# Kernel optimization log

Measured on AMD Instinct MI355X. Metric: run time of the kernel, lower is better.

The kernel has to match this reference:

```python
import jax, jax.numpy as jnp
import numpy as np

BBOX_POS_MAX = 1024.0
BN_EPS = 1e-5


def _bn_eval(x, g, b, rm, rv):
    # BatchNorm1d in eval mode: affine transform with running stats
    return g * (x - rm) * jax.lax.rsqrt(rv + BN_EPS) + b


def setup_inputs() -> dict:
    key = jax.random.key(0)
    ks = jax.random.split(key, 24)
    B, N, F = 32, 512, 1024
    E = 32768
    H1, H2, H3 = 512, 256, 128          # node_pred_hidden
    EH1, EH2 = 64, 64                   # edge_pred_hidden
    NC, EC = 8, 10                      # node/edge concept channels
    BC = 9                              # bbox_channels (4 bbox + 4 dir + 1 prio)
    s = 0.02
    inp = {
        'roi_features': jax.random.normal(ks[0], (B, N, F), jnp.float32),
        'batch_bboxes': jax.random.uniform(ks[1], (B, N, 4), jnp.float32) * BBOX_POS_MAX,
        'batch_directions': jax.random.uniform(ks[2], (B, N, 4), jnp.float32),
        'batch_priorities': jax.random.uniform(ks[3], (B, N), jnp.float32),
        'batch_edge_index': jax.random.randint(ks[4], (B, 2, E), 0, N, jnp.int32),
        # node_predictor params
        'np_w1': jax.random.normal(ks[5], (F, H1), jnp.float32) * s,
        'np_b1': jnp.zeros((H1,), jnp.float32),
        'bn1_g': jnp.ones((H1,), jnp.float32),
        'bn1_b': jnp.zeros((H1,), jnp.float32),
        'bn1_rm': jnp.zeros((H1,), jnp.float32),
        'bn1_rv': jnp.ones((H1,), jnp.float32),
        'np_w2': jax.random.normal(ks[6], (H1, H2), jnp.float32) * s,
        'np_b2': jnp.zeros((H2,), jnp.float32),
        'bn2_g': jnp.ones((H2,), jnp.float32),
        'bn2_b': jnp.zeros((H2,), jnp.float32),
        'bn2_rm': jnp.zeros((H2,), jnp.float32),
        'bn2_rv': jnp.ones((H2,), jnp.float32),
        'np_w3': jax.random.normal(ks[7], (H2, H3), jnp.float32) * s,
        'np_b3': jnp.zeros((H3,), jnp.float32),
        'ni_w': jax.random.normal(ks[8], (H3, NC), jnp.float32) * s,
        'ni_b': jnp.zeros((NC,), jnp.float32),
        # edge_predictor params (input dim = 2 * bbox_channels)
        'ep_w1': jax.random.normal(ks[9], (2 * BC, EH1), jnp.float32) * s,
        'ep_b1': jnp.zeros((EH1,), jnp.float32),
        'ep_w2': jax.random.normal(ks[10], (EH1, EH2), jnp.float32) * s,
        'ep_b2': jnp.zeros((EH2,), jnp.float32),
        'ei_w': jax.random.normal(ks[11], (EH2, EC), jnp.float32) * s,
        'ei_b': jnp.zeros((EC,), jnp.float32),
    }
    return inp


def reference(roi_features, batch_bboxes, batch_directions, batch_priorities,
              batch_edge_index,
              np_w1, np_b1, bn1_g, bn1_b, bn1_rm, bn1_rv,
              np_w2, np_b2, bn2_g, bn2_b, bn2_rm, bn2_rv,
              np_w3, np_b3, ni_w, ni_b,
              ep_w1, ep_b1, ep_w2, ep_b2, ei_w, ei_b):
    B, N, F = roi_features.shape
    # ---- node path: MLP (eval-mode BN, dropout = identity) + sigmoid interpreter
    x = roi_features.reshape(B * N, F)
    h = jax.nn.relu(_bn_eval(x @ np_w1 + np_b1, bn1_g, bn1_b, bn1_rm, bn1_rv))
    h = jax.nn.relu(_bn_eval(h @ np_w2 + np_b2, bn2_g, bn2_b, bn2_rm, bn2_rv))
    h = jax.nn.relu(h @ np_w3 + np_b3)
    node_concepts = jax.nn.sigmoid(h @ ni_w + ni_b).reshape(B, N, -1)
    # ---- edge path: per-batch gather of node attrs via edge_index, concat, MLP
    node_attr = jnp.concatenate(
        [batch_bboxes / BBOX_POS_MAX, batch_directions, batch_priorities[..., None]],
        axis=-1)  # [B, N, 9]
    C = node_attr.shape[-1]
    src_idx = batch_edge_index[:, 0, :, None]  # [B, E, 1]
    dst_idx = batch_edge_index[:, 1, :, None]
    src = jnp.take_along_axis(node_attr, src_idx.astype(jnp.int32), axis=1)  # [B, E, 9]
    dst = jnp.take_along_axis(node_attr, dst_idx.astype(jnp.int32), axis=1)
    edge_attr = jnp.concatenate([src, dst], axis=-1).reshape(-1, 2 * C)  # [B*E, 18]
    e = jax.nn.relu(edge_attr @ ep_w1 + ep_b1)
    e = jax.nn.relu(e @ ep_w2 + ep_b2)
    edge_concepts = jax.nn.sigmoid(e @ ei_w + ei_b)  # [B*E, EC]
    return node_concepts, edge_concepts
```

## Files before the change

### kernel.cpp

```cpp
#include <hip/hip_runtime.h>
#include <cstdint>
#include <cstddef>

#define BN_EPSF 1e-5f

constexpr int B_  = 32, N_ = 512, F_ = 1024, E_ = 32768;
constexpr int H1_ = 512, H2_ = 256, H3_ = 128, NC_ = 8, EC_ = 10;
constexpr int M_  = B_ * N_;
constexpr int NE_ = B_ * E_;

typedef short bf16x8 __attribute__((ext_vector_type(8)));
typedef float f32x4  __attribute__((ext_vector_type(4)));

__device__ __forceinline__ short f2bf(float f) {
  union { float f; unsigned u; } v; v.f = f;
  unsigned r = v.u + 0x7fffu + ((v.u >> 16) & 1u);
  return (short)(r >> 16);
}
__device__ __forceinline__ unsigned rnepack(float a, float b) {
  unsigned ua = __float_as_uint(a); ua = ua + 0x7fffu + ((ua >> 16) & 1u);
  unsigned ub = __float_as_uint(b); ub = ub + 0x7fffu + ((ub >> 16) & 1u);
  return __builtin_amdgcn_perm(ub, ua, 0x07060302u);
}

#define GLDS(gp, lp) __builtin_amdgcn_global_load_lds( \
    (const __attribute__((address_space(1))) void*)(gp), \
    (__attribute__((address_space(3))) void*)(lp), 16, 0, 0)

#define MFMA(a, b, c) __builtin_amdgcn_mfma_f32_16x16x32_bf16((a), (b), (c), 0, 0, 0)

__device__ __forceinline__ void wt_body(
    const float* __restrict__ W, short* __restrict__ Wt, int K, int N,
    int bx, int by, float (*s)[33])
{
  const int tx = threadIdx.x & 31, ty = threadIdx.x >> 5;
  const int k0 = by * 32, n0 = bx * 32;
#pragma unroll
  for (int r = 0; r < 4; r++)
    s[ty * 4 + r][tx] = W[(size_t)(k0 + ty * 4 + r) * N + n0 + tx];
  __syncthreads();
#pragma unroll
  for (int r = 0; r < 4; r++)
    Wt[(size_t)(n0 + ty * 4 + r) * K + k0 + tx] = f2bf(s[tx][ty * 4 + r]);
}

__global__ __launch_bounds__(256) void k_prep(
    const float* __restrict__ roi, ushort* __restrict__ roiB,
    const float* __restrict__ w1, short* __restrict__ w1t,
    const float* __restrict__ w2, short* __restrict__ w2t,
    const float* __restrict__ w3, short* __restrict__ w3t,
    const float* __restrict__ bbox, const float* __restrict__ dir,
    const float* __restrict__ pri, float* __restrict__ na)
{
  __shared__ float s[32][33];
  const int bx = blockIdx.x;
  if (bx < 8192) {
    int i = bx * 256 + threadIdx.x;
    float4 a = *(const float4*)(roi + (size_t)i * 8);
    float4 b = *(const float4*)(roi + (size_t)i * 8 + 4);
    unsigned o[4];
    o[0] = rnepack(a.x, a.y); o[1] = rnepack(a.z, a.w);
    o[2] = rnepack(b.x, b.y); o[3] = rnepack(b.z, b.w);
    *(uint4*)(roiB + (size_t)i * 8) = *(uint4*)o;
  } else if (bx < 8704) {
    int idx = bx - 8192; wt_body(w1, w1t, F_, H1_, idx & 15, idx >> 4, s);
  } else if (bx < 8832) {
    int idx = bx - 8704; wt_body(w2, w2t, H1_, H2_, idx & 7, idx >> 3, s);
  } else if (bx < 8864) {
    int idx = bx - 8832; wt_body(w3, w3t, H2_, H3_, idx & 3, idx >> 2, s);
  } else {
    int i = (bx - 8864) * 256 + threadIdx.x;
    float4 b = *(const float4*)(bbox + (size_t)i * 4);
    float4 d = *(const float4*)(dir + (size_t)i * 4);
    float p = pri[i];
    const float inv = 1.0f / 1024.0f;
    float* o = na + (size_t)i * 12;
    *(float4*)(o + 0) = make_float4(b.x * inv, b.y * inv, b.z * inv, b.w * inv);
    *(float4*)(o + 4) = make_float4(d.x, d.y, d.z, d.w);
    *(float4*)(o + 8) = make_float4(p, 0.f, 0.f, 0.f);
  }
}

__global__ __launch_bounds__(256) void k_gemm_l1(
    const short* __restrict__ A, const short* __restrict__ Wt,
    const float* __restrict__ bias,
    const float* __restrict__ g, const float* __restrict__ bb,
    const float* __restrict__ rm, const float* __restrict__ rv,
    short* __restrict__ C, int M, int K, int N)
{
  __shared__ short As[128 * 32];
  __shared__ short Bs[128 * 32];

  const int tid  = threadIdx.x;
  const int wave = tid >> 6, lane = tid & 63;
  const int m0 = blockIdx.y * 128, n0 = blockIdx.x * 128;
  const int wm = wave >> 1, wn = wave & 1;

  const int arow = tid >> 2;
  const int akq  = (tid & 3) * 8;

  f32x4 acc[4][4] = {};

  for (int k0 = 0; k0 < K; k0 += 32) {
#pragma unroll
    for (int it = 0; it < 2; it++)
      GLDS(A + (size_t)(m0 + it * 64 + arow) * K + k0 + akq,
           (char*)As + it * 4096 + wave * 1024);
#pragma unroll
    for (int it = 0; it < 2; it++)
      GLDS(Wt + (size_t)(n0 + it * 64 + arow) * K + k0 + akq,
           (char*)Bs + it * 4096 + wave * 1024);
    __syncthreads();

    const int ko = (lane >> 4) * 8;
    bf16x8 af[4], bfr[4];
#pragma unroll
    for (int t = 0; t < 4; t++) {
      af[t]  = *(const bf16x8*)&As[(wm * 64 + t * 16 + (lane & 15)) * 32 + ko];
      bfr[t] = *(const bf16x8*)&Bs[(wn * 64 + t * 16 + (lane & 15)) * 32 + ko];
    }
#pragma unroll
    for (int ti = 0; ti < 4; ti++)
#pragma unroll
      for (int tj = 0; tj < 4; tj++)
        acc[ti][tj] = MFMA(af[ti], bfr[tj], acc[ti][tj]);
    __syncthreads();
  }

#pragma unroll
  for (int tj = 0; tj < 4; tj++) {
    const int col = n0 + wn * 64 + tj * 16 + (lane & 15);
    const float bi = bias[col];
    float s = g[col] * rsqrtf(rv[col] + BN_EPSF);
    float t = bb[col] - rm[col] * s;
#pragma unroll
    for (int ti = 0; ti < 4; ti++) {
      const int rbase = m0 + wm * 64 + ti * 16 + ((lane >> 4) << 2);
#pragma unroll
      for (int r = 0; r < 4; r++) {
        float v = fmaf(acc[ti][tj][r] + bi, s, t);
        C[(size_t)(rbase + r) * N + col] = f2bf(fmaxf(v, 0.f));
      }
    }
  }
}

__global__ __launch_bounds__(256) void k_tail(
    const short* __restrict__ h1, const short* __restrict__ w2t,
    const short* __restrict__ w3t,
    const float* __restrict__ b2, const float* __restrict__ g2,
    const float* __restrict__ bb2, const float* __restrict__ rm2,
    const float* __restrict__ rv2,
    const float* __restrict__ b3, const float* __restrict__ niw,
    const float* __restrict__ nib, float* __restrict__ out)
{
  __shared__ __align__(16) char arena[53760];
  short* sA  = (short*)arena;
  short* sB  = (short*)(arena + 4096);
  short* sH2 = (short*)(arena + 36864);
  short* sB3 = (short*)arena;
  short* sH3 = (short*)(arena + 16384);

  const int tid  = threadIdx.x;
  const int wave = tid >> 6, lane = tid & 63;
  const int lm = lane & 15, q = lane >> 4;
  const int wm = wave >> 1, wn = wave & 1;
  const int m0 = blockIdx.x * 32;
  const int srow = tid >> 2;
  const int skq  = (tid & 3) * 8;

  f32x4 acc2[8] = {};
  for (int k0 = 0; k0 < 512; k0 += 64) {
    {
      int c = tid >> 7, row = (tid >> 2) & 31;
      GLDS(h1 + (size_t)(m0 + row) * 512 + k0 + c * 32 + skq,
           (char*)sA + wave * 1024);
    }
#pragma unroll
    for (int it = 0; it < 4; it++)
#pragma unroll
      for (int c = 0; c < 2; c++)
        GLDS(w2t + (size_t)(it * 64 + srow) * 512 + k0 + c * 32 + skq,
             (char*)sB + c * 16384 + it * 4096 + wave * 1024);
    __syncthreads();
#pragma unroll
    for (int c = 0; c < 2; c++) {
      bf16x8 af = *(const bf16x8*)&sA[c * 1024 + (wm * 16 + lm) * 32 + q * 8];
#pragma unroll
      for (int nt = 0; nt < 8; nt++) {
        bf16x8 bfr = *(const bf16x8*)&sB[c * 8192 + (wn * 128 + nt * 16 + lm) * 32 + q * 8];
        acc2[nt] = MFMA(af, bfr, acc2[nt]);
      }
    }
    __syncthreads();
  }
#pragma unroll
  for (int nt = 0; nt < 8; nt++) {
    int col = wn * 128 + nt * 16 + lm;
    float s = g2[col] * rsqrtf(rv2[col] + BN_EPSF);
    float t = bb2[col] - rm2[col] * s;
    float bi = b2[col];
#pragma unroll
    for (int r = 0; r < 4; r++) {
      float v = fmaf(acc2[nt][r] + bi, s, t);
      sH2[(wm * 16 + q * 4 + r) * 264 + col] = f2bf(fmaxf(v, 0.f));
    }
  }
  __syncthreads();

  f32x4 acc3[4] = {};
  for (int k0 = 0; k0 < 256; k0 += 64) {
#pragma unroll
    for (int it = 0; it < 2; it++)
#pragma unroll
      for (int c = 0; c < 2; c++)
        GLDS(w3t + (size_t)(it * 64 + srow) * 256 + k0 + c * 32 + skq,
             (char*)sB3 + c * 8192 + it * 4096 + wave * 1024);
    __syncthreads();
#pragma unroll
    for (int c = 0; c < 2; c++) {
      bf16x8 af = *(const bf16x8*)&sH2[(wm * 16 + lm) * 264 + k0 + c * 32 + q * 8];
#pragma unroll
      for (int nt = 0; nt < 4; nt++) {
        bf16x8 bfr = *(const bf16x8*)&sB3[c * 4096 + (wn * 64 + nt * 16 + lm) * 32 + q * 8];
        acc3[nt] = MFMA(af, bfr, acc3[nt]);
      }
    }
    __syncthreads();
  }
#pragma unroll
  for (int nt = 0; nt < 4; nt++) {
    int col = wn * 64 + nt * 16 + lm;
    float bi = b3[col];
#pragma unroll
    for (int r = 0; r < 4; r++) {
      float v = acc3[nt][r] + bi;
      sH3[(wm * 16 + q * 4 + r) * 136 + col] = f2bf(fmaxf(v, 0.f));
    }
  }
  __syncthreads();

  if (wave < 2) {
    f32x4 a4 = {};
#pragma unroll
    for (int c = 0; c < 4; c++) {
      ushort tmp[8];
#pragma unroll
      for (int j = 0; j < 8; j++) {
        int k = c * 32 + q * 8 + j;
        tmp[j] = (lm < 8) ? (ushort)f2bf(niw[k * 8 + lm]) : (ushort)0;
      }
      bf16x8 fw = *(bf16x8*)tmp;
      bf16x8 af4 = *(const bf16x8*)&sH3[(wave * 16 + lm) * 136 + c * 32 + q * 8];
      a4 = MFMA(af4, fw, a4);
    }
    if (lm < 8) {
      float bi = nib[lm];
#pragma unroll
      for (int r = 0; r < 4; r++) {
        float v = a4[r] + bi;
        out[(size_t)(m0 + wave * 16 + q * 4 + r) * 8 + lm] = 1.f / (1.f + __expf(-v));
      }
    }
  }
}

__global__ __launch_bounds__(256, 2) void k_edge_mfma(
    const float* __restrict__ na, const int* __restrict__ eidx,
    const float* __restrict__ w1, const float* __restrict__ b1,
    const float* __restrict__ w2, const float* __restrict__ b2,
    const float* __restrict__ wo, const float* __restrict__ bo,
    float* __restrict__ out)
{
  __shared__ __align__(16) short sA[9216];
  __shared__ __align__(16) short sH1[128 * 72];
  __shared__ float sB[144];

  const int tid  = threadIdx.x;
  const int wave = tid >> 6, lane = tid & 63;
  const int lm  = lane & 15;
  const int lk8 = (lane >> 4) * 8;
  const int lr  = (lane >> 4) * 4;

  short* sW1 = sA;
  short* sW2 = sA + 2048;
  short* sW3 = sA + 6144;
  short* sX  = sA;
  short* sH2 = sA;

  for (int i = tid; i < 2048; i += 256) {
    int n = i >> 5, k = i & 31;
    sW1[i] = (k < 18) ? f2bf(w1[k * 64 + n]) : (short)0;
  }
  for (int i = tid; i < 4096; i += 256) {
    int n = i >> 6, k = i & 63;
    sW2[i] = f2bf(w2[k * 64 + n]);
  }
  for (int i = tid; i < 1024; i += 256) {
    int n = i >> 6, k = i & 63;
    sW3[i] = (n < 10) ? f2bf(wo[k * 10 + n]) : (short)0;
  }
  if (tid < 64) { sB[tid] = b1[tid]; sB[64 + tid] = b2[tid]; }
  if (tid < 16) sB[128 + tid] = (tid < 10) ? bo[tid] : 0.f;
  __syncthreads();

  bf16x8 fW1[4], fW2[4][2], fW3[2];
#pragma unroll
  for (int t = 0; t < 4; t++)
    fW1[t] = *(const bf16x8*)&sW1[(t * 16 + lm) * 32 + lk8];
#pragma unroll
  for (int t = 0; t < 4; t++)
#pragma unroll
    for (int ks = 0; ks < 2; ks++)
      fW2[t][ks] = *(const bf16x8*)&sW2[(t * 16 + lm) * 64 + ks * 32 + lk8];
#pragma unroll
  for (int ks = 0; ks < 2; ks++)
    fW3[ks] = *(const bf16x8*)&sW3[lm * 64 + ks * 32 + lk8];
  float bias1v[4], bias2v[4];
#pragma unroll
  for (int t = 0; t < 4; t++) {
    bias1v[t] = sB[t * 16 + lm];
    bias2v[t] = sB[64 + t * 16 + lm];
  }
  const float biasOv = sB[128 + lm];
  __syncthreads();

  for (int bi = 0; bi < 4; bi++) {
    const int e0 = (blockIdx.x * 4 + bi) * 128;

    if (tid < 128) {
      int e = e0 + tid;
      int b = e >> 15, kk = e & (E_ - 1);
      const int* ei = eidx + (size_t)b * 2 * E_;
      int s = ei[kk], d = ei[E_ + kk];
      const float* ps = na + ((size_t)b * N_ + s) * 12;
      const float* pd = na + ((size_t)b * N_ + d) * 12;
      float4 a0 = *(const float4*)(ps);
      float4 a1 = *(const float4*)(ps + 4);
      float  a2 = ps[8];
      float4 c0 = *(const float4*)(pd);
      float4 c1 = *(const float4*)(pd + 4);
      float  c2 = pd[8];
      ushort xr[32];
      xr[0] = (ushort)f2bf(a0.x); xr[1] = (ushort)f2bf(a0.y);
      xr[2] = (ushort)f2bf(a0.z); xr[3] = (ushort)f2bf(a0.w);
      xr[4] = (ushort)f2bf(a1.x); xr[5] = (ushort)f2bf(a1.y);
      xr[6] = (ushort)f2bf(a1.z); xr[7] = (ushort)f2bf(a1.w);
      xr[8] = (ushort)f2bf(a2);
      xr[9]  = (ushort)f2bf(c0.x); xr[10] = (ushort)f2bf(c0.y);
      xr[11] = (ushort)f2bf(c0.z); xr[12] = (ushort)f2bf(c0.w);
      xr[13] = (ushort)f2bf(c1.x); xr[14] = (ushort)f2bf(c1.y);
      xr[15] = (ushort)f2bf(c1.z); xr[16] = (ushort)f2bf(c1.w);
      xr[17] = (ushort)f2bf(c2);
#pragma unroll
      for (int i = 18; i < 32; i++) xr[i] = 0;
      ushort* row = (ushort*)&sX[tid * 40];
      *(uint4*)(row + 0)  = *(uint4*)&xr[0];
      *(uint4*)(row + 8)  = *(uint4*)&xr[8];
      *(uint4*)(row + 16) = *(uint4*)&xr[16];
      *(uint4*)(row + 24) = *(uint4*)&xr[24];
    }
    __syncthreads();

    bf16x8 a1f[2];
#pragma unroll
    for (int ti = 0; ti < 2; ti++)
      a1f[ti] = *(const bf16x8*)&sX[(wave * 32 + ti * 16 + lm) * 40 + lk8];
    f32x4 acc1[2][4] = {};
#pragma unroll
    for (int ti = 0; ti < 2; ti++)
#pragma unroll
      for (int tj = 0; tj < 4; tj++)
        acc1[ti][tj] = MFMA(a1f[ti], fW1[tj], acc1[ti][tj]);
#pragma unroll
    for (int ti = 0; ti < 2; ti++)
#pragma unroll
      for (int tj = 0; tj < 4; tj++)
#pragma unroll
        for (int r = 0; r < 4; r++) {
          int row = wave * 32 + ti * 16 + lr + r;
          float v = acc1[ti][tj][r] + bias1v[tj];
          sH1[row * 72 + tj * 16 + lm] = f2bf(fmaxf(v, 0.f));
        }
    __syncthreads();

    bf16x8 a2f[2][2];
#pragma unroll
    for (int ti = 0; ti < 2; ti++)
#pragma unroll
      for (int ks = 0; ks < 2; ks++)
        a2f[ti][ks] = *(const bf16x8*)&sH1[(wave * 32 + ti * 16 + lm) * 72 + ks * 32 + lk8];
    f32x4 acc2[2][4] = {};
#pragma unroll
    for (int ks = 0; ks < 2; ks++)
#pragma unroll
      for (int ti = 0; ti < 2; ti++)
#pragma unroll
        for (int tj = 0; tj < 4; tj++)
          acc2[ti][tj] = MFMA(a2f[ti][ks], fW2[tj][ks], acc2[ti][tj]);
#pragma unroll
    for (int ti = 0; ti < 2; ti++)
#pragma unroll
      for (int tj = 0; tj < 4; tj++)
#pragma unroll
        for (int r = 0; r < 4; r++) {
          int row = wave * 32 + ti * 16 + lr + r;
          float v = acc2[ti][tj][r] + bias2v[tj];
          sH2[row * 72 + tj * 16 + lm] = f2bf(fmaxf(v, 0.f));
        }

    bf16x8 a3f[2][2];
#pragma unroll
    for (int ti = 0; ti < 2; ti++)
#pragma unroll
      for (int ks = 0; ks < 2; ks++)
        a3f[ti][ks] = *(const bf16x8*)&sH2[(wave * 32 + ti * 16 + lm) * 72 + ks * 32 + lk8];
    f32x4 acc3[2] = {};
#pragma unroll
    for (int ks = 0; ks < 2; ks++)
#pragma unroll
      for (int ti = 0; ti < 2; ti++)
        acc3[ti] = MFMA(a3f[ti][ks], fW3[ks], acc3[ti]);
    if (lm < 10) {
#pragma unroll
      for (int ti = 0; ti < 2; ti++)
#pragma unroll
        for (int r = 0; r < 4; r++) {
          int row = wave * 32 + ti * 16 + lr + r;
          float v = acc3[ti][r] + biasOv;
          out[(size_t)(e0 + row) * 10 + lm] = 1.f / (1.f + __expf(-v));
        }
    }
    __syncthreads();
  }
}

extern "C" void kernel_launch(void* const* d_in, const int* in_sizes, int n_in,
                              void* d_out, int out_size, void* d_ws, size_t ws_size,
                              hipStream_t stream)
{
  const float* roi   = (const float*)d_in[0];
  const float* bbox  = (const float*)d_in[1];
  const float* dir   = (const float*)d_in[2];
  const float* pri   = (const float*)d_in[3];
  const int*   eidx  = (const int*)d_in[4];
  const float* w1    = (const float*)d_in[5];
  const float* b1    = (const float*)d_in[6];
  const float* g1    = (const float*)d_in[7];
  const float* bb1   = (const float*)d_in[8];
  const float* rm1   = (const float*)d_in[9];
  const float* rv1   = (const float*)d_in[10];
  const float* w2    = (const float*)d_in[11];
  const float* b2    = (const float*)d_in[12];
  const float* g2    = (const float*)d_in[13];
  const float* bb2   = (const float*)d_in[14];
  const float* rm2   = (const float*)d_in[15];
  const float* rv2   = (const float*)d_in[16];
  const float* w3    = (const float*)d_in[17];
  const float* b3    = (const float*)d_in[18];
  const float* niw   = (const float*)d_in[19];
  const float* nib   = (const float*)d_in[20];
  const float* ew1   = (const float*)d_in[21];
  const float* eb1   = (const float*)d_in[22];
  const float* ew2   = (const float*)d_in[23];
  const float* eb2   = (const float*)d_in[24];
  const float* eow   = (const float*)d_in[25];
  const float* eob   = (const float*)d_in[26];

  float* out_node = (float*)d_out;
  float* out_edge = (float*)d_out + (size_t)M_ * NC_;

  char* w = (char*)d_ws;
  short*  roiB = (short*)w;
  short*  w1t  = (short*)(w + 33554432);
  short*  w2t  = (short*)(w + 34603008);
  short*  w3t  = (short*)(w + 34865152);
  float*  na   = (float*)(w + 34930688);
  short*  h1   = (short*)(w + 35717120);

  k_prep<<<8928, 256, 0, stream>>>(roi, (ushort*)roiB, w1, w1t, w2, w2t,
                                   w3, w3t, bbox, dir, pri, na);

  k_edge_mfma<<<NE_ / 512, 256, 0, stream>>>(
      na, eidx, ew1, eb1, ew2, eb2, eow, eob, out_edge);

  k_gemm_l1<<<dim3(H1_ / 128, M_ / 128), 256, 0, stream>>>(
      roiB, w1t, b1, g1, bb1, rm1, rv1, h1, M_, F_, H1_);
  k_tail<<<M_ / 32, 256, 0, stream>>>(
      h1, w2t, w3t, b2, g2, bb2, rm2, rv2, b3, niw, nib, out_node);
}
```

Measured before the change: 267.8 us.

## Fuse edge MLP and layer-1 GEMM into one interleaved launch with LDS node attrs

The separate edge-MLP kernel and layer-1 GEMM kernel are merged into one launch of 1536 blocks. Every third block computes a 128x128 GEMM tile, and the other two each process 1024 edges of a single batch. Edge blocks now build that batch's bf16 node attributes in LDS straight from bbox/dir/priority, which removes the node-attribute precompute in k_prep and its global scratch buffer. The aim is to overlap the memory- and latency-bound edge work with the MFMA-bound GEMM and cut one launch and a global round trip. The cost is that each edge block redoes the weight and attribute setup, and the mixed blocks share one 3-per-CU occupancy limit.

```diff
diff --git a/kernel.cpp b/kernel.cpp
--- a/kernel.cpp
+++ b/kernel.cpp
@@ -48,9 +48,7 @@
     const float* __restrict__ roi, ushort* __restrict__ roiB,
     const float* __restrict__ w1, short* __restrict__ w1t,
     const float* __restrict__ w2, short* __restrict__ w2t,
-    const float* __restrict__ w3, short* __restrict__ w3t,
-    const float* __restrict__ bbox, const float* __restrict__ dir,
-    const float* __restrict__ pri, float* __restrict__ na)
+    const float* __restrict__ w3, short* __restrict__ w3t)
 {
   __shared__ float s[32][33];
   const int bx = blockIdx.x;
@@ -66,82 +64,258 @@
     int idx = bx - 8192; wt_body(w1, w1t, F_, H1_, idx & 15, idx >> 4, s);
   } else if (bx < 8832) {
     int idx = bx - 8704; wt_body(w2, w2t, H1_, H2_, idx & 7, idx >> 3, s);
-  } else if (bx < 8864) {
+  } else {
     int idx = bx - 8832; wt_body(w3, w3t, H2_, H3_, idx & 3, idx >> 2, s);
-  } else {
-    int i = (bx - 8864) * 256 + threadIdx.x;
-    float4 b = *(const float4*)(bbox + (size_t)i * 4);
-    float4 d = *(const float4*)(dir + (size_t)i * 4);
-    float p = pri[i];
-    const float inv = 1.0f / 1024.0f;
-    float* o = na + (size_t)i * 12;
-    *(float4*)(o + 0) = make_float4(b.x * inv, b.y * inv, b.z * inv, b.w * inv);
-    *(float4*)(o + 4) = make_float4(d.x, d.y, d.z, d.w);
-    *(float4*)(o + 8) = make_float4(p, 0.f, 0.f, 0.f);
-  }
-}
-
-__global__ __launch_bounds__(256) void k_gemm_l1(
-    const short* __restrict__ A, const short* __restrict__ Wt,
-    const float* __restrict__ bias,
-    const float* __restrict__ g, const float* __restrict__ bb,
-    const float* __restrict__ rm, const float* __restrict__ rv,
-    short* __restrict__ C, int M, int K, int N)
+  }
+}
+
+__global__ __launch_bounds__(256, 3) void k_fused(
+    const float* __restrict__ bbox, const float* __restrict__ dir,
+    const float* __restrict__ pri, const int* __restrict__ eidx,
+    const float* __restrict__ ew1, const float* __restrict__ eb1,
+    const float* __restrict__ ew2, const float* __restrict__ eb2,
+    const float* __restrict__ eow, const float* __restrict__ eob,
+    float* __restrict__ out_edge,
+    const short* __restrict__ roiB, const short* __restrict__ w1t,
+    const float* __restrict__ b1, const float* __restrict__ g1,
+    const float* __restrict__ bb1, const float* __restrict__ rm1,
+    const float* __restrict__ rv1, short* __restrict__ h1)
 {
-  __shared__ short As[128 * 32];
-  __shared__ short Bs[128 * 32];
-
+  __shared__ __align__(16) char arena[49728];
+
+  const int bx = blockIdx.x;
+  const int rsel = bx % 3;
   const int tid  = threadIdx.x;
   const int wave = tid >> 6, lane = tid & 63;
-  const int m0 = blockIdx.y * 128, n0 = blockIdx.x * 128;
-  const int wm = wave >> 1, wn = wave & 1;
-
-  const int arow = tid >> 2;
-  const int akq  = (tid & 3) * 8;
-
-  f32x4 acc[4][4] = {};
-
-  for (int k0 = 0; k0 < K; k0 += 32) {
-#pragma unroll
-    for (int it = 0; it < 2; it++)
-      GLDS(A + (size_t)(m0 + it * 64 + arow) * K + k0 + akq,
-           (char*)As + it * 4096 + wave * 1024);
-#pragma unroll
-    for (int it = 0; it < 2; it++)
-      GLDS(Wt + (size_t)(n0 + it * 64 + arow) * K + k0 + akq,
-           (char*)Bs + it * 4096 + wave * 1024);
-    __syncthreads();
-
-    const int ko = (lane >> 4) * 8;
-    bf16x8 af[4], bfr[4];
-#pragma unroll
-    for (int t = 0; t < 4; t++) {
-      af[t]  = *(const bf16x8*)&As[(wm * 64 + t * 16 + (lane & 15)) * 32 + ko];
-      bfr[t] = *(const bf16x8*)&Bs[(wn * 64 + t * 16 + (lane & 15)) * 32 + ko];
-    }
-#pragma unroll
-    for (int ti = 0; ti < 4; ti++)
+  const int lm = lane & 15;
+
+  if (rsel == 2) {
+    const int lb = bx / 3;
+    short* As = (short*)arena;
+    short* Bs = (short*)(arena + 8192);
+    const int m0 = (lb >> 2) * 128, n0 = (lb & 3) * 128;
+    const int wm = wave >> 1, wn = wave & 1;
+    const int arow = tid >> 2;
+    const int akq  = (tid & 3) * 8;
+
+    f32x4 acc[4][4] = {};
+    for (int k0 = 0; k0 < F_; k0 += 32) {
+#pragma unroll
+      for (int it = 0; it < 2; it++)
+        GLDS(roiB + (size_t)(m0 + it * 64 + arow) * F_ + k0 + akq,
+             (char*)As + it * 4096 + wave * 1024);
+#pragma unroll
+      for (int it = 0; it < 2; it++)
+        GLDS(w1t + (size_t)(n0 + it * 64 + arow) * F_ + k0 + akq,
+             (char*)Bs + it * 4096 + wave * 1024);
+      __syncthreads();
+
+      const int ko = (lane >> 4) * 8;
+      bf16x8 af[4], bfr[4];
+#pragma unroll
+      for (int t = 0; t < 4; t++) {
+        af[t]  = *(const bf16x8*)&As[(wm * 64 + t * 16 + lm) * 32 + ko];
+        bfr[t] = *(const bf16x8*)&Bs[(wn * 64 + t * 16 + lm) * 32 + ko];
+      }
+#pragma unroll
+      for (int ti = 0; ti < 4; ti++)
+#pragma unroll
+        for (int tj = 0; tj < 4; tj++)
+          acc[ti][tj] = MFMA(af[ti], bfr[tj], acc[ti][tj]);
+      __syncthreads();
+    }
+#pragma unroll
+    for (int tj = 0; tj < 4; tj++) {
+      const int col = n0 + wn * 64 + tj * 16 + lm;
+      const float bi = b1[col];
+      float s = g1[col] * rsqrtf(rv1[col] + BN_EPSF);
+      float t = bb1[col] - rm1[col] * s;
+#pragma unroll
+      for (int ti = 0; ti < 4; ti++) {
+        const int rbase = m0 + wm * 64 + ti * 16 + ((lane >> 4) << 2);
+#pragma unroll
+        for (int r = 0; r < 4; r++) {
+          float v = fmaf(acc[ti][tj][r] + bi, s, t);
+          h1[(size_t)(rbase + r) * H1_ + col] = f2bf(fmaxf(v, 0.f));
+        }
+      }
+    }
+    return;
+  }
+
+  const int eb = (bx / 3) * 2 + rsel;
+  const int batch = eb >> 5;
+  const int e_base = eb * 1024;
+
+  short* sA    = (short*)arena;
+  short* sH1   = (short*)(arena + 18432);
+  ushort* sAttr= (ushort*)(arena + 36864);
+  float* sB    = (float*)(arena + 49152);
+
+  short* sW1 = sA;
+  short* sW2 = sA + 2048;
+  short* sW3 = sA + 6144;
+  short* sX  = sA;
+  short* sH2 = sA;
+
+  const int lk8 = (lane >> 4) * 8;
+  const int lr  = (lane >> 4) * 4;
+
+  for (int i = tid; i < 2048; i += 256) {
+    int n = i >> 5, k = i & 31;
+    sW1[i] = (k < 18) ? f2bf(ew1[k * 64 + n]) : (short)0;
+  }
+  for (int i = tid; i < 4096; i += 256) {
+    int n = i >> 6, k = i & 63;
+    sW2[i] = f2bf(ew2[k * 64 + n]);
+  }
+  for (int i = tid; i < 1024; i += 256) {
+    int n = i >> 6, k = i & 63;
+    sW3[i] = (n < 10) ? f2bf(eow[k * 10 + n]) : (short)0;
+  }
+  if (tid < 64) { sB[tid] = eb1[tid]; sB[64 + tid] = eb2[tid]; }
+  if (tid < 16) sB[128 + tid] = (tid < 10) ? eob[tid] : 0.f;
+  {
+    const float inv = 1.0f / 1024.0f;
+    for (int n = tid; n < 512; n += 256) {
+      int gi = batch * 512 + n;
+      float4 bv = *(const float4*)(bbox + (size_t)gi * 4);
+      float4 dv = *(const float4*)(dir + (size_t)gi * 4);
+      float pp = pri[gi];
+      unsigned* row = (unsigned*)&sAttr[n * 12];
+      uint2 a, c, e;
+      a.x = rnepack(bv.x * inv, bv.y * inv); a.y = rnepack(bv.z * inv, bv.w * inv);
+      c.x = rnepack(dv.x, dv.y);             c.y = rnepack(dv.z, dv.w);
+      e.x = rnepack(pp, 0.f);                e.y = 0;
+      *(uint2*)(row + 0) = a; *(uint2*)(row + 2) = c; *(uint2*)(row + 4) = e;
+    }
+  }
+  __syncthreads();
+
+  bf16x8 fW1[4], fW2[4][2], fW3[2];
+#pragma unroll
+  for (int t = 0; t < 4; t++)
+    fW1[t] = *(const bf16x8*)&sW1[(t * 16 + lm) * 32 + lk8];
+#pragma unroll
+  for (int t = 0; t < 4; t++)
+#pragma unroll
+    for (int ks = 0; ks < 2; ks++)
+      fW2[t][ks] = *(const bf16x8*)&sW2[(t * 16 + lm) * 64 + ks * 32 + lk8];
+#pragma unroll
+  for (int ks = 0; ks < 2; ks++)
+    fW3[ks] = *(const bf16x8*)&sW3[lm * 64 + ks * 32 + lk8];
+  float bias1v[4], bias2v[4];
+#pragma unroll
+  for (int t = 0; t < 4; t++) {
+    bias1v[t] = sB[t * 16 + lm];
+    bias2v[t] = sB[64 + t * 16 + lm];
+  }
+  const float biasOv = sB[128 + lm];
+  __syncthreads();
+
+  const int* ei = eidx + (size_t)batch * 2 * E_;
+
+  for (int bi = 0; bi < 8; bi++) {
+    const int e0 = e_base + bi * 128;
+
+    if (tid < 128) {
+      int kk = (e0 + tid) & (E_ - 1);
+      int s = ei[kk], d = ei[E_ + kk];
+      const unsigned* ps = (const unsigned*)&sAttr[s * 12];
+      const unsigned* pd = (const unsigned*)&sAttr[d * 12];
+      uint2 s01 = *(const uint2*)(ps);
+      uint2 s23 = *(const uint2*)(ps + 2);
+      uint2 s45 = *(const uint2*)(ps + 4);
+      uint2 d01 = *(const uint2*)(pd);
+      uint2 d23 = *(const uint2*)(pd + 2);
+      uint2 d45 = *(const uint2*)(pd + 4);
+      unsigned x[16];
+      x[0] = s01.x; x[1] = s01.y; x[2] = s23.x; x[3] = s23.y;
+      x[4] = (s45.x & 0xffffu) | (d01.x << 16);
+      x[5] = (d01.x >> 16) | (d01.y << 16);
+      x[6] = (d01.y >> 16) | (d23.x << 16);
+      x[7] = (d23.x >> 16) | (d23.y << 16);
+      x[8] = (d23.y >> 16) | (d45.x << 16);
+#pragma unroll
+      for (int i = 9; i < 16; i++) x[i] = 0;
+      unsigned* row = (unsigned*)&sX[tid * 40];
+      *(uint4*)(row + 0)  = *(uint4*)&x[0];
+      *(uint4*)(row + 4)  = *(uint4*)&x[4];
+      *(uint4*)(row + 8)  = *(uint4*)&x[8];
+      *(uint4*)(row + 12) = *(uint4*)&x[12];
+    }
+    __syncthreads();
+
+    bf16x8 a1f[2];
+#pragma unroll
+    for (int ti = 0; ti < 2; ti++)
+      a1f[ti] = *(const bf16x8*)&sX[(wave * 32 + ti * 16 + lm) * 40 + lk8];
+    f32x4 acc1[2][4] = {};
+#pragma unroll
+    for (int ti = 0; ti < 2; ti++)
 #pragma unroll
       for (int tj = 0; tj < 4; tj++)
-        acc[ti][tj] = MFMA(af[ti], bfr[tj], acc[ti][tj]);
-    __syncthreads();
-  }
-
-#pragma unroll
-  for (int tj = 0; tj < 4; tj++) {
-    const int col = n0 + wn * 64 + tj * 16 + (lane & 15);
-    const float bi = bias[col];
-    float s = g[col] * rsqrtf(rv[col] + BN_EPSF);
-    float t = bb[col] - rm[col] * s;
-#pragma unroll
-    for (int ti = 0; ti < 4; ti++) {
-      const int rbase = m0 + wm * 64 + ti * 16 + ((lane >> 4) << 2);
-#pragma unroll
-      for (int r = 0; r < 4; r++) {
-        float v = fmaf(acc[ti][tj][r] + bi, s, t);
-        C[(size_t)(rbase + r) * N + col] = f2bf(fmaxf(v, 0.f));
-      }
-    }
+        acc1[ti][tj] = MFMA(a1f[ti], fW1[tj], acc1[ti][tj]);
+#pragma unroll
+    for (int ti = 0; ti < 2; ti++)
+#pragma unroll
+      for (int tj = 0; tj < 4; tj++)
+#pragma unroll
+        for (int r = 0; r < 4; r++) {
+          int row = wave * 32 + ti * 16 + lr + r;
+          float v = acc1[ti][tj][r] + bias1v[tj];
+          sH1[row * 72 + tj * 16 + lm] = f2bf(fmaxf(v, 0.f));
+        }
+    __syncthreads();
+
+    bf16x8 a2f[2][2];
+#pragma unroll
+    for (int ti = 0; ti < 2; ti++)
+#pragma unroll
+      for (int ks = 0; ks < 2; ks++)
+        a2f[ti][ks] = *(const bf16x8*)&sH1[(wave * 32 + ti * 16 + lm) * 72 + ks * 32 + lk8];
+    f32x4 acc2[2][4] = {};
+#pragma unroll
+    for (int ks = 0; ks < 2; ks++)
+#pragma unroll
+      for (int ti = 0; ti < 2; ti++)
+#pragma unroll
+        for (int tj = 0; tj < 4; tj++)
+          acc2[ti][tj] = MFMA(a2f[ti][ks], fW2[tj][ks], acc2[ti][tj]);
+#pragma unroll
+    for (int ti = 0; ti < 2; ti++)
+#pragma unroll
+      for (int tj = 0; tj < 4; tj++)
+#pragma unroll
+        for (int r = 0; r < 4; r++) {
+          int row = wave * 32 + ti * 16 + lr + r;
+          float v = acc2[ti][tj][r] + bias2v[tj];
+          sH2[row * 72 + tj * 16 + lm] = f2bf(fmaxf(v, 0.f));
+        }
+
+    bf16x8 a3f[2][2];
+#pragma unroll
+    for (int ti = 0; ti < 2; ti++)
+#pragma unroll
+      for (int ks = 0; ks < 2; ks++)
+        a3f[ti][ks] = *(const bf16x8*)&sH2[(wave * 32 + ti * 16 + lm) * 72 + ks * 32 + lk8];
+    f32x4 acc3[2] = {};
+#pragma unroll
+    for (int ks = 0; ks < 2; ks++)
+#pragma unroll
+      for (int ti = 0; ti < 2; ti++)
+        acc3[ti] = MFMA(a3f[ti][ks], fW3[ks], acc3[ti]);
+    if (lm < 10) {
+#pragma unroll
+      for (int ti = 0; ti < 2; ti++)
+#pragma unroll
+        for (int r = 0; r < 4; r++) {
+          int row = wave * 32 + ti * 16 + lr + r;
+          float v = acc3[ti][r] + biasOv;
+          out_edge[(size_t)(e0 + row) * 10 + lm] = 1.f / (1.f + __expf(-v));
+        }
+    }
+    __syncthreads();
   }
 }
 
@@ -262,176 +436,6 @@
         out[(size_t)(m0 + wave * 16 + q * 4 + r) * 8 + lm] = 1.f / (1.f + __expf(-v));
       }
     }
-  }
-}
-
-__global__ __launch_bounds__(256, 2) void k_edge_mfma(
-    const float* __restrict__ na, const int* __restrict__ eidx,
-    const float* __restrict__ w1, const float* __restrict__ b1,
-    const float* __restrict__ w2, const float* __restrict__ b2,
-    const float* __restrict__ wo, const float* __restrict__ bo,
-    float* __restrict__ out)
-{
-  __shared__ __align__(16) short sA[9216];
-  __shared__ __align__(16) short sH1[128 * 72];
-  __shared__ float sB[144];
-
-  const int tid  = threadIdx.x;
-  const int wave = tid >> 6, lane = tid & 63;
-  const int lm  = lane & 15;
-  const int lk8 = (lane >> 4) * 8;
-  const int lr  = (lane >> 4) * 4;
-
-  short* sW1 = sA;
-  short* sW2 = sA + 2048;
-  short* sW3 = sA + 6144;
-  short* sX  = sA;
-  short* sH2 = sA;
-
-  for (int i = tid; i < 2048; i += 256) {
-    int n = i >> 5, k = i & 31;
-    sW1[i] = (k < 18) ? f2bf(w1[k * 64 + n]) : (short)0;
-  }
-  for (int i = tid; i < 4096; i += 256) {
-    int n = i >> 6, k = i & 63;
-    sW2[i] = f2bf(w2[k * 64 + n]);
-  }
-  for (int i = tid; i < 1024; i += 256) {
-    int n = i >> 6, k = i & 63;
-    sW3[i] = (n < 10) ? f2bf(wo[k * 10 + n]) : (short)0;
-  }
-  if (tid < 64) { sB[tid] = b1[tid]; sB[64 + tid] = b2[tid]; }
-  if (tid < 16) sB[128 + tid] = (tid < 10) ? bo[tid] : 0.f;
-  __syncthreads();
-
-  bf16x8 fW1[4], fW2[4][2], fW3[2];
-#pragma unroll
-  for (int t = 0; t < 4; t++)
-    fW1[t] = *(const bf16x8*)&sW1[(t * 16 + lm) * 32 + lk8];
-#pragma unroll
-  for (int t = 0; t < 4; t++)
-#pragma unroll
-    for (int ks = 0; ks < 2; ks++)
-      fW2[t][ks] = *(const bf16x8*)&sW2[(t * 16 + lm) * 64 + ks * 32 + lk8];
-#pragma unroll
-  for (int ks = 0; ks < 2; ks++)
-    fW3[ks] = *(const bf16x8*)&sW3[lm * 64 + ks * 32 + lk8];
-  float bias1v[4], bias2v[4];
-#pragma unroll
-  for (int t = 0; t < 4; t++) {
-    bias1v[t] = sB[t * 16 + lm];
-    bias2v[t] = sB[64 + t * 16 + lm];
-  }
-  const float biasOv = sB[128 + lm];
-  __syncthreads();
-
-  for (int bi = 0; bi < 4; bi++) {
-    const int e0 = (blockIdx.x * 4 + bi) * 128;
-
-    if (tid < 128) {
-      int e = e0 + tid;
-      int b = e >> 15, kk = e & (E_ - 1);
-      const int* ei = eidx + (size_t)b * 2 * E_;
-      int s = ei[kk], d = ei[E_ + kk];
-      const float* ps = na + ((size_t)b * N_ + s) * 12;
-      const float* pd = na + ((size_t)b * N_ + d) * 12;
-      float4 a0 = *(const float4*)(ps);
-      float4 a1 = *(const float4*)(ps + 4);
-      float  a2 = ps[8];
-      float4 c0 = *(const float4*)(pd);
-      float4 c1 = *(const float4*)(pd + 4);
-      float  c2 = pd[8];
-      ushort xr[32];
-      xr[0] = (ushort)f2bf(a0.x); xr[1] = (ushort)f2bf(a0.y);
-      xr[2] = (ushort)f2bf(a0.z); xr[3] = (ushort)f2bf(a0.w);
-      xr[4] = (ushort)f2bf(a1.x); xr[5] = (ushort)f2bf(a1.y);
-      xr[6] = (ushort)f2bf(a1.z); xr[7] = (ushort)f2bf(a1.w);
-      xr[8] = (ushort)f2bf(a2);
-      xr[9]  = (ushort)f2bf(c0.x); xr[10] = (ushort)f2bf(c0.y);
-      xr[11] = (ushort)f2bf(c0.z); xr[12] = (ushort)f2bf(c0.w);
-      xr[13] = (ushort)f2bf(c1.x); xr[14] = (ushort)f2bf(c1.y);
-      xr[15] = (ushort)f2bf(c1.z); xr[16] = (ushort)f2bf(c1.w);
-      xr[17] = (ushort)f2bf(c2);
-#pragma unroll
-      for (int i = 18; i < 32; i++) xr[i] = 0;
-      ushort* row = (ushort*)&sX[tid * 40];
-      *(uint4*)(row + 0)  = *(uint4*)&xr[0];
-      *(uint4*)(row + 8)  = *(uint4*)&xr[8];
-      *(uint4*)(row + 16) = *(uint4*)&xr[16];
-      *(uint4*)(row + 24) = *(uint4*)&xr[24];
-    }
-    __syncthreads();
-
-    bf16x8 a1f[2];
-#pragma unroll
-    for (int ti = 0; ti < 2; ti++)
-      a1f[ti] = *(const bf16x8*)&sX[(wave * 32 + ti * 16 + lm) * 40 + lk8];
-    f32x4 acc1[2][4] = {};
-#pragma unroll
-    for (int ti = 0; ti < 2; ti++)
-#pragma unroll
-      for (int tj = 0; tj < 4; tj++)
-        acc1[ti][tj] = MFMA(a1f[ti], fW1[tj], acc1[ti][tj]);
-#pragma unroll
-    for (int ti = 0; ti < 2; ti++)
-#pragma unroll
-      for (int tj = 0; tj < 4; tj++)
-#pragma unroll
-        for (int r = 0; r < 4; r++) {
-          int row = wave * 32 + ti * 16 + lr + r;
-          float v = acc1[ti][tj][r] + bias1v[tj];
-          sH1[row * 72 + tj * 16 + lm] = f2bf(fmaxf(v, 0.f));
-        }
-    __syncthreads();
-
-    bf16x8 a2f[2][2];
-#pragma unroll
-    for (int ti = 0; ti < 2; ti++)
-#pragma unroll
-      for (int ks = 0; ks < 2; ks++)
-        a2f[ti][ks] = *(const bf16x8*)&sH1[(wave * 32 + ti * 16 + lm) * 72 + ks * 32 + lk8];
-    f32x4 acc2[2][4] = {};
-#pragma unroll
-    for (int ks = 0; ks < 2; ks++)
-#pragma unroll
-      for (int ti = 0; ti < 2; ti++)
-#pragma unroll
-        for (int tj = 0; tj < 4; tj++)
-          acc2[ti][tj] = MFMA(a2f[ti][ks], fW2[tj][ks], acc2[ti][tj]);
-#pragma unroll
-    for (int ti = 0; ti < 2; ti++)
-#pragma unroll
-      for (int tj = 0; tj < 4; tj++)
-#pragma unroll
-        for (int r = 0; r < 4; r++) {
-          int row = wave * 32 + ti * 16 + lr + r;
-          float v = acc2[ti][tj][r] + bias2v[tj];
-          sH2[row * 72 + tj * 16 + lm] = f2bf(fmaxf(v, 0.f));
-        }
-
-    bf16x8 a3f[2][2];
-#pragma unroll
-    for (int ti = 0; ti < 2; ti++)
-#pragma unroll
-      for (int ks = 0; ks < 2; ks++)
-        a3f[ti][ks] = *(const bf16x8*)&sH2[(wave * 32 + ti * 16 + lm) * 72 + ks * 32 + lk8];
-    f32x4 acc3[2] = {};
-#pragma unroll
-    for (int ks = 0; ks < 2; ks++)
-#pragma unroll
-      for (int ti = 0; ti < 2; ti++)
-        acc3[ti] = MFMA(a3f[ti][ks], fW3[ks], acc3[ti]);
-    if (lm < 10) {
-#pragma unroll
-      for (int ti = 0; ti < 2; ti++)
-#pragma unroll
-        for (int r = 0; r < 4; r++) {
-          int row = wave * 32 + ti * 16 + lr + r;
-          float v = acc3[ti][r] + biasOv;
-          out[(size_t)(e0 + row) * 10 + lm] = 1.f / (1.f + __expf(-v));
-        }
-    }
-    __syncthreads();
   }
 }
 
@@ -475,17 +479,15 @@
   short*  w1t  = (short*)(w + 33554432);
   short*  w2t  = (short*)(w + 34603008);
   short*  w3t  = (short*)(w + 34865152);
-  float*  na   = (float*)(w + 34930688);
   short*  h1   = (short*)(w + 35717120);
 
-  k_prep<<<8928, 256, 0, stream>>>(roi, (ushort*)roiB, w1, w1t, w2, w2t,
-                                   w3, w3t, bbox, dir, pri, na);
-
-  k_edge_mfma<<<NE_ / 512, 256, 0, stream>>>(
-      na, eidx, ew1, eb1, ew2, eb2, eow, eob, out_edge);
-
-  k_gemm_l1<<<dim3(H1_ / 128, M_ / 128), 256, 0, stream>>>(
-      roiB, w1t, b1, g1, bb1, rm1, rv1, h1, M_, F_, H1_);
+  k_prep<<<8864, 256, 0, stream>>>(roi, (ushort*)roiB, w1, w1t, w2, w2t,
+                                   w3, w3t);
+
+  k_fused<<<1536, 256, 0, stream>>>(
+      bbox, dir, pri, eidx, ew1, eb1, ew2, eb2, eow, eob, out_edge,
+      roiB, w1t, b1, g1, bb1, rm1, rv1, h1);
+
   k_tail<<<M_ / 32, 256, 0, stream>>>(
       h1, w2t, w3t, b2, g2, bb2, rm2, rv2, b3, niw, nib, out_node);
 }
```

Result: faster. 249.6 us (-6.8%).
